# Kernel optimization log

Measured on AMD Instinct MI355X. Metric: run time of the kernel, lower is better.

Reference implementation:

```python
import jax, jax.numpy as jnp
import numpy as np


def setup_inputs() -> dict:
    key = jax.random.key(0)
    k_x, k_m, k_w1, k_b1, k_w2, k_b2 = jax.random.split(key, 6)
    b, seq_len, d_in, d_out = 8, 4096, 1024, 512
    x = jax.random.normal(k_x, (b, seq_len, d_in), dtype=jnp.float32)
    # binary-ish mask in {0,1} as floats (torch code multiplies by mask)
    mask = (jax.random.uniform(k_m, (b, seq_len)) < 0.5).astype(jnp.float32)
    s1 = 1.0 / np.sqrt(d_in)
    s2 = 1.0 / np.sqrt(d_out)
    W_enc = jax.random.uniform(k_w1, (d_out, d_in), minval=-s1, maxval=s1, dtype=jnp.float32)
    b_enc = jax.random.uniform(k_b1, (d_out,), minval=-s1, maxval=s1, dtype=jnp.float32)
    W_dec = jax.random.uniform(k_w2, (d_in, d_out), minval=-s2, maxval=s2, dtype=jnp.float32)
    b_dec = jax.random.uniform(k_b2, (d_in,), minval=-s2, maxval=s2, dtype=jnp.float32)
    return {"x": x, "mask": mask, "W_enc": W_enc, "b_enc": b_enc, "W_dec": W_dec, "b_dec": b_dec}


def reference(x, mask, W_enc, b_enc, W_dec, b_dec):
    # per-step: v_t = v_{t-1} + relu(x_t @ W_enc^T + b_enc) * mask_t  -> additive scan == cumsum
    h = jax.nn.relu(jnp.einsum('bsd,od->bso', x, W_enc) + b_enc) * mask[:, :, None]  # [b,s,d_out]
    v_cum = jnp.cumsum(h, axis=1)  # [b,s,d_out]
    out_enc = jnp.einsum('bso,do->bsd', v_cum, W_dec) + b_dec  # decode every prefix state
    v = v_cum[:, -1, :]  # final accumulated state
    return (v, out_enc)
```

## Files before the change

### kernel.cpp

```cpp
#include <hip/hip_runtime.h>
#include <hip/hip_bf16.h>
#include <stdint.h>

typedef __bf16 bf16_t;
typedef __bf16 bf16x4 __attribute__((ext_vector_type(4)));
typedef __bf16 bf16x8 __attribute__((ext_vector_type(8)));
typedef float  f32x4  __attribute__((ext_vector_type(4)));

__device__ __forceinline__ void gload_lds16(const void* g, void* l) {
  __builtin_amdgcn_global_load_lds(
      (__attribute__((address_space(1))) void*)g,
      (__attribute__((address_space(3))) void*)l, 16, 0, 0);
}

__global__ void cast_all(const float* __restrict__ x, bf16_t* __restrict__ xb,
                         const float* __restrict__ we, bf16_t* __restrict__ web,
                         const float* __restrict__ wd, bf16_t* __restrict__ wdb) {
  const int NX = 8388608;
  const int NW = 131072;
  const int stride = gridDim.x * blockDim.x;
  for (int i = blockIdx.x * blockDim.x + threadIdx.x; i < NX + 2 * NW; i += stride) {
    const float* src; bf16_t* dst; int k;
    if (i < NX)           { src = x;  dst = xb;  k = i; }
    else if (i < NX + NW) { src = we; dst = web; k = i - NX; }
    else                  { src = wd; dst = wdb; k = i - NX - NW; }
    f32x4 v = reinterpret_cast<const f32x4*>(src)[k];
    bf16x4 o;
    o[0] = (bf16_t)v[0]; o[1] = (bf16_t)v[1]; o[2] = (bf16_t)v[2]; o[3] = (bf16_t)v[3];
    reinterpret_cast<bf16x4*>(dst)[k] = o;
  }
}

#define PHASE_SYNC() do { \
  __builtin_amdgcn_s_barrier(); \
  asm volatile("s_waitcnt lgkmcnt(0)" ::: "memory"); \
  __builtin_amdgcn_sched_barrier(0); \
  __builtin_amdgcn_s_setprio(1); \
} while (0)

#define PHASE_END() do { \
  __builtin_amdgcn_s_setprio(0); \
  __builtin_amdgcn_s_barrier(); \
} while (0)

#define QUAD(RH, CH, BF) do { \
  _Pragma("unroll") \
  for (int fr = 0; fr < 4; ++fr) { \
    _Pragma("unroll") \
    for (int fc = 0; fc < 2; ++fc) { \
      acc[RH][CH][fr][fc] = __builtin_amdgcn_mfma_f32_16x16x32_bf16(a[fr][0], BF[fc][0], acc[RH][CH][fr][fc], 0, 0, 0); \
      acc[RH][CH][fr][fc] = __builtin_amdgcn_mfma_f32_16x16x32_bf16(a[fr][1], BF[fc][1], acc[RH][CH][fr][fc], 0, 0, 0); \
    } \
  } \
} while (0)

template<int EPI>
__global__ __launch_bounds__(512, 2) void gemm8p(
    const bf16_t* __restrict__ A, const bf16_t* __restrict__ B,
    const int K, const int N,
    const float* __restrict__ bias, const float* __restrict__ mask,
    const float* __restrict__ Padd,
    bf16_t* __restrict__ h_out, float* __restrict__ partials,
    float* __restrict__ outf)
{
  __shared__ __align__(16) char smem[131072];

  const int tid  = threadIdx.x;
  const int lane = tid & 63;
  const int w    = tid >> 6;
  const int wm   = w >> 2;
  const int wn   = w & 3;
  const long bm  = (long)blockIdx.x * 256;
  const long bn  = (long)blockIdx.y * 256;
  const int NT   = K >> 6;

  const int scol = (((lane & 7) ^ (lane >> 3)) << 3);
  const int fcb0 = ((((lane >> 4)    ) ^ (lane & 7)) << 3);
  const int fcb1 = ((((lane >> 4) + 4) ^ (lane & 7)) << 3);

  f32x4  acc[2][2][4][2] = {};
  bf16x8 a[4][2], b0[2][2], b1[2][2];

  auto Albs = [&](int buf) { return (bf16_t*)(smem + buf * 65536); };
  auto Blbs = [&](int buf) { return (bf16_t*)(smem + buf * 65536 + 32768); };

  auto stageA = [&](int t, int h) {
    bf16_t* lb = Albs(t & 1);
    #pragma unroll
    for (int c = 0; c < 2; ++c) {
      const int r0 = h * 128 + (w * 2 + c) * 8;
      gload_lds16(A + (bm + r0 + (lane >> 3)) * (long)K + t * 64 + scol, lb + r0 * 64);
    }
  };
  auto stageB = [&](int t, int h) {
    bf16_t* lb = Blbs(t & 1);
    #pragma unroll
    for (int c = 0; c < 2; ++c) {
      const int r0 = h * 128 + (w * 2 + c) * 8;
      gload_lds16(B + (bn + r0 + (lane >> 3)) * (long)K + t * 64 + scol, lb + r0 * 64);
    }
  };
  auto loadA = [&](int buf, int rh) {
    const bf16_t* lb = Albs(buf);
    #pragma unroll
    for (int fr = 0; fr < 4; ++fr) {
      const int row = rh * 128 + wm * 64 + fr * 16 + (lane & 15);
      a[fr][0] = *reinterpret_cast<const bf16x8*>(lb + row * 64 + fcb0);
      a[fr][1] = *reinterpret_cast<const bf16x8*>(lb + row * 64 + fcb1);
    }
  };
  auto loadB = [&](int buf, int ch, bf16x8 (&bf)[2][2]) {
    const bf16_t* lb = Blbs(buf);
    #pragma unroll
    for (int fc = 0; fc < 2; ++fc) {
      const int row = ch * 128 + wn * 32 + fc * 16 + (lane & 15);
      bf[fc][0] = *reinterpret_cast<const bf16x8*>(lb + row * 64 + fcb0);
      bf[fc][1] = *reinterpret_cast<const bf16x8*>(lb + row * 64 + fcb1);
    }
  };

  __builtin_amdgcn_sched_barrier(0);
  stageA(0, 0); stageA(0, 1); stageB(0, 0); stageB(0, 1);
  stageA(1, 0); stageA(1, 1); stageB(1, 0); stageB(1, 1);
  asm volatile("s_waitcnt vmcnt(8)" ::: "memory");
  __builtin_amdgcn_s_barrier();

  for (int t = 0; t < NT; ++t) {
    const int buf = t & 1;
    const bool g2 = (t + 2 < NT);

    loadA(buf, 0); loadB(buf, 0, b0);
    asm volatile("s_waitcnt lgkmcnt(8)" ::: "memory");
    PHASE_SYNC(); QUAD(0, 0, b0); PHASE_END();

    loadB(buf, 1, b1);
    if (g2) stageA(t + 2, 0);
    PHASE_SYNC(); QUAD(0, 1, b1); PHASE_END();

    loadA(buf, 1);
    if (g2) stageB(t + 2, 0);
    PHASE_SYNC(); QUAD(1, 0, b0); PHASE_END();

    if (g2) { stageA(t + 2, 1); stageB(t + 2, 1); }
    PHASE_SYNC(); QUAD(1, 1, b1);
    __builtin_amdgcn_s_setprio(0);
    if (g2) asm volatile("s_waitcnt vmcnt(8)" ::: "memory");
    else    asm volatile("s_waitcnt vmcnt(0)" ::: "memory");
    __builtin_amdgcn_s_barrier();
  }
  __builtin_amdgcn_sched_barrier(0);

  if (EPI == 0) {
    bf16_t* tile = (bf16_t*)smem;
    float bv[2][2];
    #pragma unroll
    for (int ch = 0; ch < 2; ++ch)
      #pragma unroll
      for (int fc = 0; fc < 2; ++fc)
        bv[ch][fc] = bias[bn + ch * 128 + wn * 32 + fc * 16 + (lane & 15)];

    #pragma unroll
    for (int rh = 0; rh < 2; ++rh)
      #pragma unroll
      for (int fr = 0; fr < 4; ++fr) {
        const int row0 = rh * 128 + wm * 64 + fr * 16 + ((lane >> 4) << 2);
        const f32x4 mv = *reinterpret_cast<const f32x4*>(&mask[bm + row0]);
        #pragma unroll
        for (int ch = 0; ch < 2; ++ch)
          #pragma unroll
          for (int fc = 0; fc < 2; ++fc) {
            const int col = ch * 128 + wn * 32 + fc * 16 + (lane & 15);
            #pragma unroll
            for (int e = 0; e < 4; ++e) {
              const int row = row0 + e;
              float hv = acc[rh][ch][fr][fc][e] + bv[ch][fc];
              hv = (hv > 0.f ? hv : 0.f) * mv[e];
              tile[row * 256 + (col ^ (((row >> 2) & 3) << 4))] = (bf16_t)hv;
            }
          }
      }
    __syncthreads();

    const int sub = tid >> 8;
    const int col = tid & 255;
    float run = 0.f;
    bf16_t* hp = h_out + (bm + sub * 128) * 512 + bn + col;
    #pragma unroll 4
    for (int s = 0; s < 128; ++s) {
      const int row = sub * 128 + s;
      run += (float)tile[row * 256 + (col ^ (((row >> 2) & 3) << 4))];
      hp[(long)s * 512] = (bf16_t)run;
    }
    partials[(blockIdx.x * 2 + sub) * 512 + bn + col] = run;
  } else {
    #pragma unroll
    for (int rh = 0; rh < 2; ++rh)
      #pragma unroll
      for (int ch = 0; ch < 2; ++ch)
        #pragma unroll
        for (int fc = 0; fc < 2; ++fc) {
          const long gc = bn + ch * 128 + wn * 32 + fc * 16 + (lane & 15);
          const float pv = Padd[(blockIdx.x * 2 + rh) * (long)N + gc];
          #pragma unroll
          for (int fr = 0; fr < 4; ++fr) {
            const long gr = bm + rh * 128 + wm * 64 + fr * 16 + ((lane >> 4) << 2);
            #pragma unroll
            for (int e = 0; e < 4; ++e)
              outf[(gr + e) * (long)N + gc] = acc[rh][ch][fr][fc][e] + pv;
          }
        }
  }
}

__global__ __launch_bounds__(256) void gemm_p(
    const bf16_t* __restrict__ A, const bf16_t* __restrict__ B,
    const int K, const int N,
    const float* __restrict__ bias,
    float* __restrict__ outf)
{
  __shared__ __align__(16) bf16_t As[2][128 * 64];
  __shared__ __align__(16) bf16_t Bs[2][128 * 64];

  const int tid  = threadIdx.x;
  const int lane = tid & 63;
  const int w    = tid >> 6;
  const int wm   = w >> 1, wn = w & 1;
  const long bm  = (long)blockIdx.x * 128;
  const long bn  = (long)blockIdx.y * 128;

  f32x4 acc[4][4] = {};

  const int srow = w * 32 + (lane >> 3);
  const int scol = (lane & 7) * 8;
  const bf16_t* Abase = A + (bm + srow) * (long)K + scol;
  const bf16_t* Bbase = B + (bn + srow) * (long)K + scol;

  auto stage = [&](bf16_t* da, bf16_t* db, int kt) {
    #pragma unroll
    for (int it = 0; it < 4; ++it) {
      gload_lds16(Abase + (long)it * 8 * K + kt, &da[(w * 32 + it * 8) * 64]);
      gload_lds16(Bbase + (long)it * 8 * K + kt, &db[(w * 32 + it * 8) * 64]);
    }
  };
  auto mfma_tile = [&](const bf16_t* Asb, const bf16_t* Bsb) {
    #pragma unroll
    for (int kk = 0; kk < 2; ++kk) {
      const int kof = kk * 32 + (lane >> 4) * 8;
      bf16x8 afr[4], bfr[4];
      #pragma unroll
      for (int i = 0; i < 4; ++i)
        afr[i] = *reinterpret_cast<const bf16x8*>(&Asb[(wm * 64 + i * 16 + (lane & 15)) * 64 + kof]);
      #pragma unroll
      for (int j = 0; j < 4; ++j)
        bfr[j] = *reinterpret_cast<const bf16x8*>(&Bsb[(wn * 64 + j * 16 + (lane & 15)) * 64 + kof]);
      #pragma unroll
      for (int i = 0; i < 4; ++i)
        #pragma unroll
        for (int j = 0; j < 4; ++j)
          acc[i][j] = __builtin_amdgcn_mfma_f32_16x16x32_bf16(afr[i], bfr[j], acc[i][j], 0, 0, 0);
    }
  };

  stage(As[0], Bs[0], 0);
  __syncthreads();
  int kt = 64;
  for (int p2 = 0; p2 < (K >> 7); ++p2) {
    if (kt < K) stage(As[1], Bs[1], kt);
    mfma_tile(As[0], Bs[0]);
    __syncthreads();
    kt += 64;
    if (kt < K) stage(As[0], Bs[0], kt);
    mfma_tile(As[1], Bs[1]);
    __syncthreads();
    kt += 64;
  }

  #pragma unroll
  for (int j = 0; j < 4; ++j) {
    const long gc = bn + wn * 64 + j * 16 + (lane & 15);
    const float addv = bias[gc];
    #pragma unroll
    for (int i = 0; i < 4; ++i) {
      const long gr0 = bm + wm * 64 + i * 16 + ((lane >> 4) << 2);
      #pragma unroll
      for (int r = 0; r < 4; ++r)
        outf[(gr0 + r) * (long)N + gc] = acc[i][j][r] + addv;
    }
  }
}

__global__ void scan_chunks(const float* __restrict__ partials, bf16_t* __restrict__ prefixb,
                            float* __restrict__ v_out) {
  const int idx = blockIdx.x * blockDim.x + threadIdx.x;
  const int b = idx >> 9;
  const int o = idx & 511;
  float run = 0.f;
  #pragma unroll
  for (int c = 0; c < 32; ++c) {
    const size_t off = ((size_t)(b * 32 + c)) * 512 + o;
    prefixb[off] = (bf16_t)run;
    run += partials[off];
  }
  v_out[idx] = run;
}

extern "C" void kernel_launch(void* const* d_in, const int* in_sizes, int n_in,
                              void* d_out, int out_size, void* d_ws, size_t ws_size,
                              hipStream_t stream) {
  const float* x     = (const float*)d_in[0];
  const float* mask  = (const float*)d_in[1];
  const float* W_enc = (const float*)d_in[2];
  const float* b_enc = (const float*)d_in[3];
  const float* W_dec = (const float*)d_in[4];
  const float* b_dec = (const float*)d_in[5];

  float* out     = (float*)d_out;
  float* v_out   = out;
  float* out_enc = out + 4096;

  char* ws = (char*)d_ws;
  bf16_t* xb       = (bf16_t*)ws;  ws += (size_t)32768 * 1024 * 2;
  bf16_t* Web      = (bf16_t*)ws;  ws += (size_t)512 * 1024 * 2;
  bf16_t* Wdb      = (bf16_t*)ws;  ws += (size_t)1024 * 512 * 2;
  bf16_t* h        = (bf16_t*)ws;  ws += (size_t)32768 * 512 * 2;
  float*  partials = (float*)ws;   ws += (size_t)256 * 512 * 4;
  bf16_t* prefixb  = (bf16_t*)ws;  ws += (size_t)256 * 512 * 2;
  float*  P        = (float*)ws;   ws += (size_t)256 * 1024 * 4;

  cast_all<<<2048, 256, 0, stream>>>(x, xb, W_enc, Web, W_dec, Wdb);

  gemm8p<0><<<dim3(128, 2), 512, 0, stream>>>(xb, Web, 1024, 512,
                                              b_enc, mask, nullptr, h, partials, nullptr);

  scan_chunks<<<16, 256, 0, stream>>>(partials, prefixb, v_out);

  gemm_p<<<dim3(2, 8), 256, 0, stream>>>(prefixb, Wdb, 512, 1024, b_dec, P);

  gemm8p<1><<<dim3(128, 4), 512, 0, stream>>>(h, Wdb, 512, 1024,
                                              nullptr, nullptr, P, nullptr, nullptr, out_enc);
}
```

Measured before the change: 162.0 us.

## Fuse fp32-to-bf16 cast of x into the encoder GEMM with full-width N tiles

```diff
diff --git a/kernel.cpp b/kernel.cpp
--- a/kernel.cpp
+++ b/kernel.cpp
@@ -13,21 +13,157 @@
       (__attribute__((address_space(3))) void*)l, 16, 0, 0);
 }
 
-__global__ void cast_all(const float* __restrict__ x, bf16_t* __restrict__ xb,
-                         const float* __restrict__ we, bf16_t* __restrict__ web,
-                         const float* __restrict__ wd, bf16_t* __restrict__ wdb) {
-  const int NX = 8388608;
-  const int NW = 131072;
-  const int stride = gridDim.x * blockDim.x;
-  for (int i = blockIdx.x * blockDim.x + threadIdx.x; i < NX + 2 * NW; i += stride) {
-    const float* src; bf16_t* dst; int k;
-    if (i < NX)           { src = x;  dst = xb;  k = i; }
-    else if (i < NX + NW) { src = we; dst = web; k = i - NX; }
-    else                  { src = wd; dst = wdb; k = i - NX - NW; }
-    f32x4 v = reinterpret_cast<const f32x4*>(src)[k];
-    bf16x4 o;
-    o[0] = (bf16_t)v[0]; o[1] = (bf16_t)v[1]; o[2] = (bf16_t)v[2]; o[3] = (bf16_t)v[3];
-    reinterpret_cast<bf16x4*>(dst)[k] = o;
+__global__ void cast_weights(const float* __restrict__ a, bf16_t* __restrict__ oa,
+                             const float* __restrict__ b, bf16_t* __restrict__ ob,
+                             int n4each) {
+  const int i = blockIdx.x * blockDim.x + threadIdx.x;
+  const float* src; bf16_t* dst; int k;
+  if (i < n4each) { src = a; dst = oa; k = i; }
+  else            { src = b; dst = ob; k = i - n4each; }
+  f32x4 v = reinterpret_cast<const f32x4*>(src)[k];
+  bf16x4 o;
+  o[0] = (bf16_t)v[0]; o[1] = (bf16_t)v[1]; o[2] = (bf16_t)v[2]; o[3] = (bf16_t)v[3];
+  reinterpret_cast<bf16x4*>(dst)[k] = o;
+}
+
+__global__ __launch_bounds__(512, 2) void gemm1_fn(
+    const float* __restrict__ x, const bf16_t* __restrict__ Wenc,
+    const float* __restrict__ b_enc, const float* __restrict__ mask,
+    bf16_t* __restrict__ h_out, float* __restrict__ partials)
+{
+  __shared__ __align__(16) char smem[131072];
+  auto Al = [&](int buf) { return (bf16_t*)(smem + buf * 8192); };
+  auto Bl = [&](int buf) { return (bf16_t*)(smem + 16384 + buf * 32768); };
+
+  const int tid  = threadIdx.x;
+  const int lane = tid & 63;
+  const int w    = tid >> 6;
+  const int wm   = w >> 2;
+  const int wn   = w & 3;
+  const long bm  = (long)blockIdx.x * 128;
+  const int NT   = 32;
+
+  f32x4  acc[4][8] = {};
+  bf16x8 a[4], b[8];
+  f32x4  av0[2], av1[2];
+
+  const int arow = tid >> 2;
+  const int ab   = tid & 3;
+  auto gaLoad = [&](int t, f32x4 (&av)[2]) {
+    const float* s = x + (bm + arow) * 1024 + t * 32 + ab * 8;
+    av[0] = *reinterpret_cast<const f32x4*>(s);
+    av[1] = *reinterpret_cast<const f32x4*>(s + 4);
+  };
+  auto aWrite = [&](int buf, const f32x4 (&av)[2]) {
+    bf16x8 o;
+    #pragma unroll
+    for (int e = 0; e < 4; ++e) { o[e] = (bf16_t)av[0][e]; o[e + 4] = (bf16_t)av[1][e]; }
+    const int eb = ab ^ ((arow >> 1) & 3);
+    *reinterpret_cast<bf16x8*>(Al(buf) + arow * 32 + eb * 8) = o;
+  };
+
+  auto stageB = [&](int t, int buf) {
+    bf16_t* lb = Bl(buf);
+    #pragma unroll
+    for (int it = 0; it < 4; ++it) {
+      const int r0  = w * 64 + it * 16;
+      const int row = r0 + (lane >> 2);
+      const int kqs = (lane & 3) ^ ((row >> 1) & 3);
+      gload_lds16(Wenc + row * 1024 + t * 32 + kqs * 8, lb + r0 * 32);
+    }
+  };
+
+  const int kq = lane >> 4;
+  auto mfma_tile = [&](int buf) {
+    const bf16_t* Asb = Al(buf);
+    const bf16_t* Bsb = Bl(buf);
+    #pragma unroll
+    for (int fr = 0; fr < 4; ++fr) {
+      const int row = wm * 64 + fr * 16 + (lane & 15);
+      a[fr] = *reinterpret_cast<const bf16x8*>(Asb + row * 32 + ((kq ^ ((row >> 1) & 3)) * 8));
+    }
+    #pragma unroll
+    for (int fn = 0; fn < 8; ++fn) {
+      const int row = wn * 128 + fn * 16 + (lane & 15);
+      b[fn] = *reinterpret_cast<const bf16x8*>(Bsb + row * 32 + ((kq ^ ((row >> 1) & 3)) * 8));
+    }
+    #pragma unroll
+    for (int fr = 0; fr < 4; ++fr)
+      #pragma unroll
+      for (int fn = 0; fn < 8; ++fn)
+        acc[fr][fn] = __builtin_amdgcn_mfma_f32_16x16x32_bf16(a[fr], b[fn], acc[fr][fn], 0, 0, 0);
+  };
+
+  stageB(0, 0);
+  gaLoad(0, av0);
+  gaLoad(1, av1);
+  aWrite(0, av0);
+  asm volatile("s_waitcnt vmcnt(0) lgkmcnt(0)" ::: "memory");
+  __builtin_amdgcn_s_barrier();
+
+  for (int t = 0; t < NT; t += 2) {
+    {
+      const bool g1 = (t + 1 < NT), g2 = (t + 2 < NT);
+      if (g1) stageB(t + 1, 1);
+      if (g2) gaLoad(t + 2, av0);
+      mfma_tile(0);
+      if (g1) {
+        aWrite(1, av1);
+        if (g2) asm volatile("s_waitcnt vmcnt(2) lgkmcnt(0)" ::: "memory");
+        else    asm volatile("s_waitcnt vmcnt(0) lgkmcnt(0)" ::: "memory");
+        __builtin_amdgcn_s_barrier();
+      }
+    }
+    {
+      const bool g1 = (t + 1 < NT), g2 = (t + 2 < NT), g3 = (t + 3 < NT);
+      if (g2) stageB(t + 2, 0);
+      if (g3) gaLoad(t + 3, av1);
+      if (g1) mfma_tile(1);
+      if (g2) {
+        aWrite(0, av0);
+        if (g3) asm volatile("s_waitcnt vmcnt(2) lgkmcnt(0)" ::: "memory");
+        else    asm volatile("s_waitcnt vmcnt(0) lgkmcnt(0)" ::: "memory");
+        __builtin_amdgcn_s_barrier();
+      }
+    }
+  }
+  asm volatile("s_waitcnt vmcnt(0) lgkmcnt(0)" ::: "memory");
+  __builtin_amdgcn_s_barrier();
+
+  bf16_t* tile = (bf16_t*)smem;
+  float bv[8];
+  #pragma unroll
+  for (int fn = 0; fn < 8; ++fn)
+    bv[fn] = b_enc[wn * 128 + fn * 16 + (lane & 15)];
+
+  #pragma unroll
+  for (int fr = 0; fr < 4; ++fr) {
+    const int row0 = wm * 64 + fr * 16 + ((lane >> 4) << 2);
+    const f32x4 mv = *reinterpret_cast<const f32x4*>(&mask[bm + row0]);
+    #pragma unroll
+    for (int fn = 0; fn < 8; ++fn) {
+      const int col = wn * 128 + fn * 16 + (lane & 15);
+      #pragma unroll
+      for (int e = 0; e < 4; ++e) {
+        const int row = row0 + e;
+        float hv = acc[fr][fn][e] + bv[fn];
+        hv = (hv > 0.f ? hv : 0.f) * mv[e];
+        tile[row * 512 + (col ^ ((row & 3) << 4))] = (bf16_t)hv;
+      }
+    }
+  }
+  __syncthreads();
+
+  {
+    const int col = tid;
+    float run = 0.f;
+    bf16_t* hp = h_out + bm * 512 + col;
+    #pragma unroll 4
+    for (int r = 0; r < 128; ++r) {
+      run += (float)tile[r * 512 + (col ^ ((r & 3) << 4))];
+      hp[(long)r * 512] = (bf16_t)run;
+    }
+    partials[blockIdx.x * 512 + col] = run;
   }
 }
 
@@ -54,13 +190,10 @@
   } \
 } while (0)
 
-template<int EPI>
-__global__ __launch_bounds__(512, 2) void gemm8p(
+__global__ __launch_bounds__(512, 2) void gemm2_8p(
     const bf16_t* __restrict__ A, const bf16_t* __restrict__ B,
     const int K, const int N,
-    const float* __restrict__ bias, const float* __restrict__ mask,
     const float* __restrict__ Padd,
-    bf16_t* __restrict__ h_out, float* __restrict__ partials,
     float* __restrict__ outf)
 {
   __shared__ __align__(16) char smem[131072];
@@ -130,7 +263,6 @@
     const bool g2 = (t + 2 < NT);
 
     loadA(buf, 0); loadB(buf, 0, b0);
-    asm volatile("s_waitcnt lgkmcnt(8)" ::: "memory");
     PHASE_SYNC(); QUAD(0, 0, b0); PHASE_END();
 
     loadB(buf, 1, b1);
@@ -150,66 +282,22 @@
   }
   __builtin_amdgcn_sched_barrier(0);
 
-  if (EPI == 0) {
-    bf16_t* tile = (bf16_t*)smem;
-    float bv[2][2];
+  #pragma unroll
+  for (int rh = 0; rh < 2; ++rh)
     #pragma unroll
     for (int ch = 0; ch < 2; ++ch)
       #pragma unroll
-      for (int fc = 0; fc < 2; ++fc)
-        bv[ch][fc] = bias[bn + ch * 128 + wn * 32 + fc * 16 + (lane & 15)];
-
-    #pragma unroll
-    for (int rh = 0; rh < 2; ++rh)
-      #pragma unroll
-      for (int fr = 0; fr < 4; ++fr) {
-        const int row0 = rh * 128 + wm * 64 + fr * 16 + ((lane >> 4) << 2);
-        const f32x4 mv = *reinterpret_cast<const f32x4*>(&mask[bm + row0]);
+      for (int fc = 0; fc < 2; ++fc) {
+        const long gc = bn + ch * 128 + wn * 32 + fc * 16 + (lane & 15);
+        const float pv = Padd[(blockIdx.x * 2 + rh) * (long)N + gc];
         #pragma unroll
-        for (int ch = 0; ch < 2; ++ch)
+        for (int fr = 0; fr < 4; ++fr) {
+          const long gr = bm + rh * 128 + wm * 64 + fr * 16 + ((lane >> 4) << 2);
           #pragma unroll
-          for (int fc = 0; fc < 2; ++fc) {
-            const int col = ch * 128 + wn * 32 + fc * 16 + (lane & 15);
-            #pragma unroll
-            for (int e = 0; e < 4; ++e) {
-              const int row = row0 + e;
-              float hv = acc[rh][ch][fr][fc][e] + bv[ch][fc];
-              hv = (hv > 0.f ? hv : 0.f) * mv[e];
-              tile[row * 256 + (col ^ (((row >> 2) & 3) << 4))] = (bf16_t)hv;
-            }
-          }
+          for (int e = 0; e < 4; ++e)
+            outf[(gr + e) * (long)N + gc] = acc[rh][ch][fr][fc][e] + pv;
+        }
       }
-    __syncthreads();
-
-    const int sub = tid >> 8;
-    const int col = tid & 255;
-    float run = 0.f;
-    bf16_t* hp = h_out + (bm + sub * 128) * 512 + bn + col;
-    #pragma unroll 4
-    for (int s = 0; s < 128; ++s) {
-      const int row = sub * 128 + s;
-      run += (float)tile[row * 256 + (col ^ (((row >> 2) & 3) << 4))];
-      hp[(long)s * 512] = (bf16_t)run;
-    }
-    partials[(blockIdx.x * 2 + sub) * 512 + bn + col] = run;
-  } else {
-    #pragma unroll
-    for (int rh = 0; rh < 2; ++rh)
-      #pragma unroll
-      for (int ch = 0; ch < 2; ++ch)
-        #pragma unroll
-        for (int fc = 0; fc < 2; ++fc) {
-          const long gc = bn + ch * 128 + wn * 32 + fc * 16 + (lane & 15);
-          const float pv = Padd[(blockIdx.x * 2 + rh) * (long)N + gc];
-          #pragma unroll
-          for (int fr = 0; fr < 4; ++fr) {
-            const long gr = bm + rh * 128 + wm * 64 + fr * 16 + ((lane >> 4) << 2);
-            #pragma unroll
-            for (int e = 0; e < 4; ++e)
-              outf[(gr + e) * (long)N + gc] = acc[rh][ch][fr][fc][e] + pv;
-          }
-        }
-  }
 }
 
 __global__ __launch_bounds__(256) void gemm_p(
@@ -319,7 +407,6 @@
   float* out_enc = out + 4096;
 
   char* ws = (char*)d_ws;
-  bf16_t* xb       = (bf16_t*)ws;  ws += (size_t)32768 * 1024 * 2;
   bf16_t* Web      = (bf16_t*)ws;  ws += (size_t)512 * 1024 * 2;
   bf16_t* Wdb      = (bf16_t*)ws;  ws += (size_t)1024 * 512 * 2;
   bf16_t* h        = (bf16_t*)ws;  ws += (size_t)32768 * 512 * 2;
@@ -327,15 +414,13 @@
   bf16_t* prefixb  = (bf16_t*)ws;  ws += (size_t)256 * 512 * 2;
   float*  P        = (float*)ws;   ws += (size_t)256 * 1024 * 4;
 
-  cast_all<<<2048, 256, 0, stream>>>(x, xb, W_enc, Web, W_dec, Wdb);
-
-  gemm8p<0><<<dim3(128, 2), 512, 0, stream>>>(xb, Web, 1024, 512,
-                                              b_enc, mask, nullptr, h, partials, nullptr);
+  cast_weights<<<1024, 256, 0, stream>>>(W_enc, Web, W_dec, Wdb, 131072);
+
+  gemm1_fn<<<dim3(256, 1), 512, 0, stream>>>(x, Web, b_enc, mask, h, partials);
 
   scan_chunks<<<16, 256, 0, stream>>>(partials, prefixb, v_out);
 
   gemm_p<<<dim3(2, 8), 256, 0, stream>>>(prefixb, Wdb, 512, 1024, b_dec, P);
 
-  gemm8p<1><<<dim3(128, 4), 512, 0, stream>>>(h, Wdb, 512, 1024,
-                                              nullptr, nullptr, P, nullptr, nullptr, out_enc);
-}
+  gemm2_8p<<<dim3(128, 4), 512, 0, stream>>>(h, Wdb, 512, 1024, P, out_enc);
+}
```

Result: faster. 138.9 us (-14.3%).
